# Performance work log

Measured on AMD Instinct MI355X. Metric: run time of the kernel, lower is better.

The kernel has to match this reference:

```python
import jax, jax.numpy as jnp
import numpy as np

B, S, C, P, E = 8, 16, 32, 64, 768       # batch, max_spans, max_cand, max_prop, emb_dim
M = S * C                                 # bags per batch = 512
L = M * P                                 # triplet ids per batch = 32768
T = 100000                                # triplet vocab size
NE = 1000000                              # num_entities


def setup_inputs() -> dict:
    key = jax.random.key(0)
    k0, k1, k2, k3, k4, k5 = jax.random.split(key, 6)
    span_embs = jax.random.normal(k0, (B, S, E), dtype=jnp.float32)
    triplet_ids_tr = jax.random.randint(k1, (B, L), 0, T, dtype=jnp.int32)
    # uniform bags: bag i covers [i*P, (i+1)*P); offsets must start at 0 (EmbeddingBag)
    offsets_tr = jnp.tile(jnp.arange(M, dtype=jnp.int32) * P, (B, 1))
    attention_tr = jax.random.uniform(k2, (B, L), dtype=jnp.float32)
    qid_inds = jax.random.randint(k3, (B, M), 0, NE + 1, dtype=jnp.int32)
    emb_weight = jax.random.normal(k4, (T, E), dtype=jnp.float32) * 0.02
    span_W = jax.random.normal(k5, (E, 1), dtype=jnp.float32) * 0.02
    span_b = jnp.zeros((1,), dtype=jnp.float32)
    return {"span_embs": span_embs, "triplet_ids_tr": triplet_ids_tr,
            "offsets_tr": offsets_tr, "attention_tr": attention_tr,
            "qid_inds": qid_inds, "emb_weight": emb_weight,
            "span_W": span_W, "span_b": span_b}


def _embedding_bag_sum(ids, offs, w, table):
    # ids,w: [L]; offs: [M] sorted, offs[0]==0 -> sum-pooled bags [M, E]
    pos = jnp.arange(ids.shape[0])
    seg = jnp.searchsorted(offs, pos, side='right') - 1  # bag id per element
    gathered = table[ids] * w[:, None]                    # [L, E]
    return jax.ops.segment_sum(gathered, seg, num_segments=M)


def reference(span_embs, triplet_ids_tr, offsets_tr, attention_tr, qid_inds,
              emb_weight, span_W, span_b):
    span_scores = span_embs @ span_W + span_b              # [B, S, 1]
    # torch repeat(1, max_cand, 1): whole span block tiled C times along dim 1
    exp_emb = jnp.tile(span_embs, (1, C, 1))               # [B, C*S, E]
    kb_embs = jax.vmap(_embedding_bag_sum, in_axes=(0, 0, 0, None))(
        triplet_ids_tr, offsets_tr, attention_tr, emb_weight)  # [B, M, E]
    mult1 = (kb_embs * exp_emb).reshape(B, S, C, E)
    sum1 = jnp.sum(mult1, axis=3)                          # [B, S, C]
    sm1 = jax.nn.softmax(sum1, axis=1)                     # softmax over spans
    mult2 = (span_scores * sm1).reshape(B, S * C)
    cand_scores = jax.nn.softmax(mult2, axis=1)            # [B, M]
    # one-hot matmul == scatter-add of cand scores onto entity ids
    scatter = jax.vmap(lambda q, s: jnp.zeros(NE + 1, dtype=s.dtype).at[q].add(s))(
        qid_inds, cand_scores)                             # [B, NE+1]
    x0 = scatter[:, :-1, None]                             # drop padding entity -> [B, NE, 1]
    return jax.nn.softmax(x0, axis=1)
```

## Files before the change

kernel.cpp:

```cpp
#include <hip/hip_runtime.h>

#define B   8
#define S   16
#define C   32
#define P   64
#define E   768
#define M   512
#define LL  32768
#define NE  1000000
#define TR  100000
#define KI  24

typedef __attribute__((ext_vector_type(8))) short short8;
typedef __attribute__((ext_vector_type(4))) float f32x4;

__device__ __forceinline__ short f2bf(float x) {
    unsigned u = __float_as_uint(x);
    u += 0x7FFFu + ((u >> 16) & 1u);
    return (short)(u >> 16);
}

__device__ __forceinline__ short8 pack8(float4 lo, float4 hi) {
    short8 r;
    r[0] = f2bf(lo.x); r[1] = f2bf(lo.y); r[2] = f2bf(lo.z); r[3] = f2bf(lo.w);
    r[4] = f2bf(hi.x); r[5] = f2bf(hi.y); r[6] = f2bf(hi.z); r[7] = f2bf(hi.w);
    return r;
}

__global__ __launch_bounds__(256) void k_pre_bfrag(
    const float* __restrict__ span, short8* __restrict__ bfrag)
{
    const int idx = blockIdx.x * 256 + threadIdx.x;
    if (idx >= KI * 8 * 64) return;
    const int lane = idx & 63;
    const int ct   = (idx >> 6) & 7;
    const int kk   = idx >> 9;
    const int n = ct * 16 + (lane & 15);
    const int k = kk * 32 + (lane >> 4) * 8;
    const float* sp = span + (size_t)n * E + k;
    const float4 lo = *(const float4*)sp;
    const float4 hi = *(const float4*)(sp + 4);
    bfrag[idx] = pack8(lo, hi);
}

__global__ __launch_bounds__(256, 3) void k0_dot_table(
    const float* __restrict__ emb,
    const short8* __restrict__ bfrag,
    float*       __restrict__ dt)
{
    const int tid  = threadIdx.x;
    const int wave = tid >> 6;
    const int lane = tid & 63;
    const int mrow = lane & 15;
    const int kq   = lane >> 4;
    const int rbase = blockIdx.x * 128;

    __shared__ short8 Abuf[2][8][64];

    const int srow  = tid >> 3;
    const int kpart = tid & 7;
    const int dlane = (kpart >> 1) * 16;
    const int dsub  = (kpart & 1) * 4;

    f32x4 acc[2][8];
    #pragma unroll
    for (int i = 0; i < 2; ++i)
        #pragma unroll
        for (int j = 0; j < 8; ++j)
            acc[i][j] = f32x4{0.f, 0.f, 0.f, 0.f};

    #pragma unroll
    for (int p = 0; p < 4; ++p) {
        const int row  = p * 32 + srow;
        int grow = rbase + row; if (grow >= TR) grow = TR - 1;
        const float4 v = *(const float4*)(emb + (size_t)grow * E + kpart * 4);
        short* dst = (short*)&Abuf[0][row >> 4][dlane + (row & 15)] + dsub;
        dst[0] = f2bf(v.x); dst[1] = f2bf(v.y); dst[2] = f2bf(v.z); dst[3] = f2bf(v.w);
    }
    __syncthreads();

    for (int kk = 0; kk < KI; ++kk) {
        const int buf = kk & 1;

        const short8 A0 = Abuf[buf][wave * 2][lane];
        const short8 A1 = Abuf[buf][wave * 2 + 1][lane];

        short8 Bf[8];
        #pragma unroll
        for (int ct = 0; ct < 8; ++ct)
            Bf[ct] = bfrag[(kk * 8 + ct) * 64 + lane];

        float4 nv[4];
        if (kk + 1 < KI) {
            #pragma unroll
            for (int p = 0; p < 4; ++p) {
                const int row = p * 32 + srow;
                int grow = rbase + row; if (grow >= TR) grow = TR - 1;
                nv[p] = *(const float4*)(emb + (size_t)grow * E + (kk + 1) * 32 + kpart * 4);
            }
        }

        #pragma unroll
        for (int ct = 0; ct < 8; ++ct) {
            acc[0][ct] = __builtin_amdgcn_mfma_f32_16x16x32_bf16(A0, Bf[ct], acc[0][ct], 0, 0, 0);
            acc[1][ct] = __builtin_amdgcn_mfma_f32_16x16x32_bf16(A1, Bf[ct], acc[1][ct], 0, 0, 0);
        }

        if (kk + 1 < KI) {
            #pragma unroll
            for (int p = 0; p < 4; ++p) {
                const int row = p * 32 + srow;
                short* dst = (short*)&Abuf[buf ^ 1][row >> 4][dlane + (row & 15)] + dsub;
                dst[0] = f2bf(nv[p].x); dst[1] = f2bf(nv[p].y);
                dst[2] = f2bf(nv[p].z); dst[3] = f2bf(nv[p].w);
            }
        }
        __syncthreads();
    }

    #pragma unroll
    for (int rt = 0; rt < 2; ++rt) {
        const int orow = rbase + (wave * 2 + rt) * 16 + kq * 4;
        #pragma unroll
        for (int r = 0; r < 4; ++r) {
            if (orow + r < TR) {
                float* o = dt + (size_t)(orow + r) * 128 + mrow;
                #pragma unroll
                for (int ct = 0; ct < 8; ++ct) o[ct * 16] = acc[rt][ct][r];
            }
        }
    }
}

__global__ __launch_bounds__(256) void k1_bagdot(
    const float* __restrict__ dt,
    const int*   __restrict__ ids,
    const float* __restrict__ att,
    float*       __restrict__ sum1)
{
    const int seg  = blockIdx.x * 4 + (threadIdx.x >> 6);
    const int lane = threadIdx.x & 63;
    const int b = seg >> 9;
    const int m = seg & 511;
    const int n = (b << 4) | (m & 15);

    const size_t base = (size_t)b * LL + (size_t)m * P;
    const int   id = ids[base + lane];
    const float a  = att[base + lane];
    float v = a * dt[(size_t)id * 128 + n];

    #pragma unroll
    for (int off = 32; off > 0; off >>= 1)
        v += __shfl_down(v, off, 64);
    if (lane == 0) sum1[seg] = v;
}

__global__ __launch_bounds__(512) void k2_fused(
    const float* __restrict__ sum1,
    const float* __restrict__ span,
    const float* __restrict__ spanW,
    const float* __restrict__ spanb,
    const int*   __restrict__ qids,
    float*       __restrict__ sval,
    float*       __restrict__ invden)
{
    const int b = blockIdx.x;
    const int t = threadIdx.x;

    __shared__ float ls[512];
    __shared__ float cs[512];
    __shared__ int   qs[512];
    __shared__ float ss[16];
    __shared__ float inv_s;

    {
        const int s = t >> 5, j = t & 31;
        const float* sp = span + (size_t)(b * S + s) * E;
        float partial = 0.f;
        for (int e = j; e < E; e += 32) partial = fmaf(sp[e], spanW[e], partial);
        #pragma unroll
        for (int off = 16; off > 0; off >>= 1) partial += __shfl_down(partial, off, 32);
        if (j == 0) ss[s] = partial + spanb[0];
    }

    const float v = sum1[b * M + t];
    ls[t] = v;
    qs[t] = qids[b * M + t];
    __syncthreads();

    const int c = t & 31;
    float mx = -1e30f;
    #pragma unroll
    for (int s2 = 0; s2 < S; ++s2) mx = fmaxf(mx, ls[s2 * 32 + c]);
    float den = 0.f;
    #pragma unroll
    for (int s2 = 0; s2 < S; ++s2) den += expf(ls[s2 * 32 + c] - mx);
    const float m2 = ss[t >> 5] * (expf(v - mx) / den);
    __syncthreads();

    ls[t] = m2; __syncthreads();
    for (int off = 256; off > 0; off >>= 1) {
        if (t < off) ls[t] = fmaxf(ls[t], ls[t + off]);
        __syncthreads();
    }
    const float bigM = ls[0];
    __syncthreads();
    const float ex = expf(m2 - bigM);
    ls[t] = ex; __syncthreads();
    for (int off = 256; off > 0; off >>= 1) {
        if (t < off) ls[t] += ls[t + off];
        __syncthreads();
    }
    const float cand = ex / ls[0];
    __syncthreads();

    cs[t] = cand; __syncthreads();

    const int myq = qs[t];
    float dsum = 0.f;
    int first = 512;
    #pragma unroll 8
    for (int j = 0; j < 512; ++j) {
        const bool match = (qs[j] == myq);
        dsum += match ? cs[j] : 0.f;
        if (match && j < first) first = j;
    }
    const bool owner = (first == t) && (myq < NE);
    const float ev = owner ? expf(dsum) : 1.f;

    ls[t] = owner ? (ev - 1.f) : 0.f;
    __syncthreads();
    for (int off = 256; off > 0; off >>= 1) {
        if (t < off) ls[t] += ls[t + off];
        __syncthreads();
    }
    if (t == 0) {
        const float iv = 1.f / (1.0e6f + ls[0]);
        invden[b] = iv;
        inv_s = iv;
    }
    __syncthreads();

    sval[b * M + t] = owner ? ev * inv_s : 0.f;
}

__global__ __launch_bounds__(256) void k3_fill(
    float* __restrict__ out, const float* __restrict__ invden)
{
    const int i = blockIdx.x * 256 + threadIdx.x;
    if (i >= (B * NE) / 4) return;
    const float v = invden[i / (NE / 4)];
    reinterpret_cast<float4*>(out)[i] = make_float4(v, v, v, v);
}

__global__ __launch_bounds__(512) void k4_scatter(
    const float* __restrict__ sval, const int* __restrict__ qids,
    float* __restrict__ out)
{
    const int b = blockIdx.x, t = threadIdx.x;
    const float v = sval[b * M + t];
    const int   q = qids[b * M + t];
    if (v > 0.f && q < NE) out[(size_t)b * NE + q] = v;
}

extern "C" void kernel_launch(void* const* d_in, const int* in_sizes, int n_in,
                              void* d_out, int out_size, void* d_ws, size_t ws_size,
                              hipStream_t stream)
{
    (void)in_sizes; (void)n_in; (void)out_size; (void)ws_size;

    const float* span_embs = (const float*)d_in[0];
    const int*   ids       = (const int*)  d_in[1];
    const float* att       = (const float*)d_in[3];
    const int*   qids      = (const int*)  d_in[4];
    const float* emb       = (const float*)d_in[5];
    const float* spanW     = (const float*)d_in[6];
    const float* spanb     = (const float*)d_in[7];

    float* out = (float*)d_out;

    float*  dt     = (float*)d_ws;
    float*  sum1   = dt + (size_t)TR * 128;
    float*  sval   = sum1 + B * M;
    float*  invden = sval + B * M;
    short8* bfrag  = (short8*)(invden + 64);

    k_pre_bfrag<<<(KI * 8 * 64 + 255) / 256, 256, 0, stream>>>(span_embs, bfrag);
    k0_dot_table<<<(TR + 127) / 128, 256, 0, stream>>>(emb, bfrag, dt);
    k1_bagdot<<<(B * M) / 4, 256, 0, stream>>>(dt, ids, att, sum1);
    k2_fused<<<B, 512, 0, stream>>>(sum1, span_embs, spanW, spanb, qids, sval, invden);
    k3_fill<<<((B * NE / 4) + 255) / 256, 256, 0, stream>>>(out, invden);
    k4_scatter<<<B, 512, 0, stream>>>(sval, qids, out);
}
```

Measured before the change: 523.8 us.

## Stream embedding tiles directly into LDS with global_load_lds and XOR swizzle

The dot-table kernel now loads fp32 embedding tiles straight from global memory into shared memory using the async global_load_lds builtin, instead of loading them through registers and converting to bf16 before storing. The bf16 packing moves to the consumer side after the LDS read, and an XOR swizzle on the column index is meant to avoid bank conflicts. Each wave now owns a contiguous 32-row slab. This is meant to cut register pressure and VALU work in the producer path and overlap the prefetch with the MFMAs, at the cost of doubling LDS footprint (fp32) and repeating the bf16 conversion per wave.

```diff
diff --git a/kernel.cpp b/kernel.cpp
--- a/kernel.cpp
+++ b/kernel.cpp
@@ -25,6 +25,13 @@
     r[0] = f2bf(lo.x); r[1] = f2bf(lo.y); r[2] = f2bf(lo.z); r[3] = f2bf(lo.w);
     r[4] = f2bf(hi.x); r[5] = f2bf(hi.y); r[6] = f2bf(hi.z); r[7] = f2bf(hi.w);
     return r;
+}
+
+__device__ __forceinline__ void gl_lds16(const float* g, float* l) {
+    __builtin_amdgcn_global_load_lds(
+        (const __attribute__((address_space(1))) unsigned int*)g,
+        (__attribute__((address_space(3))) unsigned int*)l,
+        16, 0, 0);
 }
 
 __global__ __launch_bounds__(256) void k_pre_bfrag(
@@ -48,6 +55,8 @@
     const short8* __restrict__ bfrag,
     float*       __restrict__ dt)
 {
+    __shared__ float Abuf[2][128][32];
+
     const int tid  = threadIdx.x;
     const int wave = tid >> 6;
     const int lane = tid & 63;
@@ -55,12 +64,20 @@
     const int kq   = lane >> 4;
     const int rbase = blockIdx.x * 128;
 
-    __shared__ short8 Abuf[2][8][64];
-
-    const int srow  = tid >> 3;
-    const int kpart = tid & 7;
-    const int dlane = (kpart >> 1) * 16;
-    const int dsub  = (kpart & 1) * 4;
+    const int srow = lane >> 3;
+    const int sc16 = (lane & 7) ^ srow;
+    const float* gb[4];
+    #pragma unroll
+    for (int p = 0; p < 4; ++p) {
+        int rg = rbase + wave * 32 + p * 8 + srow;
+        if (rg >= TR) rg = TR - 1;
+        gb[p] = emb + (size_t)rg * E + sc16 * 4;
+    }
+
+    const int r7 = mrow & 7;
+    const int f0 = (wave * 32 + mrow) * 32 + (((kq * 2)     ^ r7) << 2);
+    const int f1 = (wave * 32 + mrow) * 32 + (((kq * 2 + 1) ^ r7) << 2);
+    const float* Af = &Abuf[0][0][0];
 
     f32x4 acc[2][8];
     #pragma unroll
@@ -70,35 +87,31 @@
             acc[i][j] = f32x4{0.f, 0.f, 0.f, 0.f};
 
     #pragma unroll
-    for (int p = 0; p < 4; ++p) {
-        const int row  = p * 32 + srow;
-        int grow = rbase + row; if (grow >= TR) grow = TR - 1;
-        const float4 v = *(const float4*)(emb + (size_t)grow * E + kpart * 4);
-        short* dst = (short*)&Abuf[0][row >> 4][dlane + (row & 15)] + dsub;
-        dst[0] = f2bf(v.x); dst[1] = f2bf(v.y); dst[2] = f2bf(v.z); dst[3] = f2bf(v.w);
-    }
+    for (int p = 0; p < 4; ++p)
+        gl_lds16(gb[p], &Abuf[0][wave * 32 + p * 8][0]);
     __syncthreads();
 
     for (int kk = 0; kk < KI; ++kk) {
         const int buf = kk & 1;
 
-        const short8 A0 = Abuf[buf][wave * 2][lane];
-        const short8 A1 = Abuf[buf][wave * 2 + 1][lane];
+        if (kk + 1 < KI) {
+            #pragma unroll
+            for (int p = 0; p < 4; ++p)
+                gl_lds16(gb[p] + (kk + 1) * 32, &Abuf[buf ^ 1][wave * 32 + p * 8][0]);
+        }
+
+        const float* Ab = Af + buf * 4096;
+        const float4 x0 = *(const float4*)(Ab + f0);
+        const float4 x1 = *(const float4*)(Ab + f1);
+        const float4 y0 = *(const float4*)(Ab + f0 + 512);
+        const float4 y1 = *(const float4*)(Ab + f1 + 512);
+        const short8 A0 = pack8(x0, x1);
+        const short8 A1 = pack8(y0, y1);
 
         short8 Bf[8];
         #pragma unroll
         for (int ct = 0; ct < 8; ++ct)
             Bf[ct] = bfrag[(kk * 8 + ct) * 64 + lane];
-
-        float4 nv[4];
-        if (kk + 1 < KI) {
-            #pragma unroll
-            for (int p = 0; p < 4; ++p) {
-                const int row = p * 32 + srow;
-                int grow = rbase + row; if (grow >= TR) grow = TR - 1;
-                nv[p] = *(const float4*)(emb + (size_t)grow * E + (kk + 1) * 32 + kpart * 4);
-            }
-        }
 
         #pragma unroll
         for (int ct = 0; ct < 8; ++ct) {
@@ -106,21 +119,12 @@
             acc[1][ct] = __builtin_amdgcn_mfma_f32_16x16x32_bf16(A1, Bf[ct], acc[1][ct], 0, 0, 0);
         }
 
-        if (kk + 1 < KI) {
-            #pragma unroll
-            for (int p = 0; p < 4; ++p) {
-                const int row = p * 32 + srow;
-                short* dst = (short*)&Abuf[buf ^ 1][row >> 4][dlane + (row & 15)] + dsub;
-                dst[0] = f2bf(nv[p].x); dst[1] = f2bf(nv[p].y);
-                dst[2] = f2bf(nv[p].z); dst[3] = f2bf(nv[p].w);
-            }
-        }
         __syncthreads();
     }
 
     #pragma unroll
     for (int rt = 0; rt < 2; ++rt) {
-        const int orow = rbase + (wave * 2 + rt) * 16 + kq * 4;
+        const int orow = rbase + wave * 32 + rt * 16 + kq * 4;
         #pragma unroll
         for (int r = 0; r < 4; ++r) {
             if (orow + r < TR) {
```

Result: no change. 521.2 us (-0.5%).
